# Performance work log

Measured on AMD Instinct MI355X. Metric: run time of the kernel, lower is better.

## Reference

```python
import jax, jax.numpy as jnp
import numpy as np

MAX_POS = 8192
SOFT_CAP = 5.0


def rms_norm(x, scale, eps=1e-6):
    # RMSBatchNorm approximated as RMS normalization over channels with learned scale
    return x * jax.lax.rsqrt(jnp.mean(x * x, axis=-1, keepdims=True) + eps) * scale


def layer_norm(x, scale, offset, eps=1e-5):
    mean = jnp.mean(x, axis=-1, keepdims=True)
    var = jnp.mean(jnp.square(x - mean), axis=-1, keepdims=True)
    return (x - mean) * jax.lax.rsqrt(var + eps) * scale + offset


def apply_rope(x, max_position=MAX_POS):
    # x: [B, S, H, C]
    B, S, H, C = x.shape
    positions = jnp.arange(S, dtype=x.dtype).reshape(1, S)
    num_freq = C // 2
    inv_freq = (1.0 / (jnp.arange(num_freq) + jnp.geomspace(1, max_position - num_freq + 1, num_freq))).astype(x.dtype)
    theta = jnp.einsum('bs,f->bsf', positions, inv_freq)
    theta = jnp.repeat(theta, 2, axis=-1)[..., None, :]  # [1, S, 1, C]
    x_rotated = jnp.stack([-x[..., 1::2], x[..., ::2]], axis=-1).reshape(x.shape)
    return x * jnp.cos(theta) + x_rotated * jnp.sin(theta)


def setup_inputs() -> dict:
    key = jax.random.key(0)
    ks = jax.random.split(key, 16)
    B, S, D = 2, 2048, 1536
    H, CQK, CV = 8, 128, 192
    inp = {
        'x': jax.random.normal(ks[0], (B, S, D), jnp.float32),
        'attention_bias': jax.random.normal(ks[1], (B, H, S, S), jnp.float32),
        'rms_in_scale': jnp.ones((D,), jnp.float32),
        'wq': jax.random.normal(ks[2], (D, H * CQK), jnp.float32) / np.sqrt(D),
        'wk': jax.random.normal(ks[3], (D, CQK), jnp.float32) / np.sqrt(D),
        'wv': jax.random.normal(ks[4], (D, CV), jnp.float32) / np.sqrt(D),
        'q_scale': jnp.ones((CQK,), jnp.float32),
        'q_offset': jnp.zeros((CQK,), jnp.float32),
        'k_scale': jnp.ones((CQK,), jnp.float32),
        'k_offset': jnp.zeros((CQK,), jnp.float32),
        'v_scale': jnp.ones((CV,), jnp.float32),
        'v_offset': jnp.zeros((CV,), jnp.float32),
        'wo': jax.random.normal(ks[5], (H * CV, D), jnp.float32) / np.sqrt(H * CV),
        'bo': jnp.zeros((D,), jnp.float32),
        'rms_out_scale': jnp.ones((D,), jnp.float32),
    }
    return inp


def reference(x, attention_bias, rms_in_scale, wq, wk, wv, q_scale, q_offset,
              k_scale, k_offset, v_scale, v_offset, wo, bo, rms_out_scale):
    B, S, D = x.shape
    H, CQK, CV = 8, 128, 192
    h = rms_norm(x, rms_in_scale)
    q = layer_norm((h @ wq).reshape(B, S, H, CQK), q_scale, q_offset)
    k = layer_norm((h @ wk).reshape(B, S, 1, CQK), k_scale, k_offset)
    v = layer_norm((h @ wv).reshape(B, S, 1, CV), v_scale, v_offset)
    q = apply_rope(q)
    k = apply_rope(k)
    # MQA logits: single shared K head
    logits = jnp.einsum('bshc,bSc->bhsS', q, k[:, :, 0], preferred_element_type=jnp.float32)
    logits = logits / np.sqrt(128.0)
    logits = (logits + attention_bias).astype(jnp.float32)
    logits = jnp.tanh(logits / SOFT_CAP) * SOFT_CAP
    weights = jax.nn.softmax(logits, axis=-1)
    y = jnp.einsum('bhsS,bSc->bshc', weights, v[:, :, 0]).astype(q.dtype)
    y = y.reshape(B, S, H * CV) @ wo + bo
    return rms_norm(y, rms_out_scale)
```

## Files before the change

### kernel.cpp

```cpp
#include <hip/hip_runtime.h>
#include <hip/hip_bf16.h>

typedef unsigned short u16;
typedef short bf16x8 __attribute__((ext_vector_type(8)));
typedef float f32x4 __attribute__((ext_vector_type(4)));

#define NB 2
#define NS 2048
#define ND 1536
#define NH 8
#define NCQK 128
#define NCV 192
#define NBS 4096
#define NPAD 1408

__device__ __forceinline__ float bf2f(u16 u) {
  unsigned v = ((unsigned)u) << 16;
  return __builtin_bit_cast(float, v);
}
__device__ __forceinline__ u16 f2bf(float f) {
  unsigned u = __builtin_bit_cast(unsigned, f);
  u += 0x7fffu + ((u >> 16) & 1u);
  return (u16)(u >> 16);
}
__device__ __forceinline__ void glds16(const u16* g, u16* l) {
  __builtin_amdgcn_global_load_lds(
      (const __attribute__((address_space(1))) void*)g,
      (__attribute__((address_space(3))) void*)l, 16, 0, 0);
}
__device__ __forceinline__ f32x4 mfma16(bf16x8 a, bf16x8 b, f32x4 c) {
  return __builtin_amdgcn_mfma_f32_16x16x32_bf16(a, b, c, 0, 0, 0);
}

__global__ void transpose_k(const float* __restrict__ in, u16* __restrict__ out,
                            int K, int N) {
  __shared__ float t[64][65];
  const int n0 = blockIdx.x * 64, k0 = blockIdx.y * 64;
  const int tid = threadIdx.x;
  const int rl = tid >> 4, cl = (tid & 15) * 4;
  for (int p = 0; p < 4; p++) {
    int k = rl + p * 16;
    float4 v = *(const float4*)(in + (size_t)(k0 + k) * N + n0 + cl);
    t[k][cl] = v.x; t[k][cl + 1] = v.y; t[k][cl + 2] = v.z; t[k][cl + 3] = v.w;
  }
  __syncthreads();
  const int rn = tid >> 3, ck = (tid & 7) * 8;
  for (int p = 0; p < 2; p++) {
    int n = rn + p * 32;
    u16 tmp[8];
    for (int j = 0; j < 8; j++) tmp[j] = f2bf(t[ck + j][n]);
    *(uint4*)(out + (size_t)(n0 + n) * K + k0 + ck) = *(uint4*)tmp;
  }
}

__global__ void rmsnorm_in_k(const float* __restrict__ x, const float* __restrict__ scale,
                             u16* __restrict__ h) {
  __shared__ float sbuf[4];
  const int row = blockIdx.x, tid = threadIdx.x;
  const float* xr = x + (size_t)row * ND;
  float v[6]; float ss = 0.f;
  for (int i = 0; i < 6; i++) { v[i] = xr[tid + i * 256]; ss += v[i] * v[i]; }
  for (int o = 32; o; o >>= 1) ss += __shfl_xor(ss, o);
  if ((tid & 63) == 0) sbuf[tid >> 6] = ss;
  __syncthreads();
  ss = sbuf[0] + sbuf[1] + sbuf[2] + sbuf[3];
  const float inv = rsqrtf(ss * (1.f / ND) + 1e-6f);
  u16* hr = h + (size_t)row * ND;
  for (int i = 0; i < 6; i++) {
    int c = tid + i * 256;
    hr[c] = f2bf(v[i] * inv * scale[c]);
  }
}

template <bool F32OUT>
__global__ __launch_bounds__(256, 2)
void gemm_nt(const u16* __restrict__ A, const u16* __restrict__ Bt,
             float* __restrict__ Cf, u16* __restrict__ Cb, int M, int N, int K) {
  __shared__ __align__(16) u16 As[128 * 64];
  __shared__ __align__(16) u16 Bs[128 * 64];
  const int tid = threadIdx.x;
  const int wave = tid >> 6, lane = tid & 63, quad = lane >> 4, l16 = lane & 15;
  const int m0 = blockIdx.y * 128, n0 = blockIdx.x * 128;
  const int mrb = (wave & 1) * 4, nrb = (wave >> 1) * 4;
  f32x4 acc[4][4] = {};
  for (int k0 = 0; k0 < K; k0 += 64) {
    if (k0) __syncthreads();
    for (int i = 0; i < 4; i++) {
      int g = wave * 4 + i;
      int rb = g >> 1, kh = g & 1;
      int row = rb * 16 + l16, kc = kh * 4 + quad;
      glds16(A + (size_t)(m0 + row) * K + k0 + kc * 8, &As[(rb * 8 + kh * 4) * 128]);
      glds16(Bt + (size_t)(n0 + row) * K + k0 + kc * 8, &Bs[(rb * 8 + kh * 4) * 128]);
    }
    __syncthreads();
    for (int kk = 0; kk < 2; kk++) {
      bf16x8 af[4], bfr[4];
      for (int f = 0; f < 4; f++)
        af[f] = *(const bf16x8*)&As[(((mrb + f) * 8 + kk * 4 + quad) * 16 + l16) * 8];
      for (int f = 0; f < 4; f++)
        bfr[f] = *(const bf16x8*)&Bs[(((nrb + f) * 8 + kk * 4 + quad) * 16 + l16) * 8];
      for (int mf = 0; mf < 4; mf++)
        for (int nf = 0; nf < 4; nf++)
          acc[mf][nf] = mfma16(af[mf], bfr[nf], acc[mf][nf]);
    }
  }
  for (int mf = 0; mf < 4; mf++)
    for (int nf = 0; nf < 4; nf++)
      for (int r = 0; r < 4; r++) {
        int m = m0 + (wave & 1) * 64 + mf * 16 + quad * 4 + r;
        int n = n0 + (wave >> 1) * 64 + nf * 16 + l16;
        if (F32OUT) Cf[(size_t)m * N + n] = acc[mf][nf][r];
        else        Cb[(size_t)m * N + n] = f2bf(acc[mf][nf][r]);
      }
}

__global__ void ln_rope_k(const float* __restrict__ qkv,
                          const float* __restrict__ qs, const float* __restrict__ qo,
                          const float* __restrict__ ks, const float* __restrict__ ko,
                          const float* __restrict__ vs, const float* __restrict__ vo,
                          u16* __restrict__ Qg, u16* __restrict__ Kg, u16* __restrict__ Vg) {
  const int row = blockIdx.x;
  const int b = row >> 11, s = row & (NS - 1);
  const int wave = threadIdx.x >> 6, lane = threadIdx.x & 63;
  const float* base = qkv + (size_t)row * NPAD;
  const float gsp = __expf(logf(8129.f) * ((float)lane * (1.f / 63.f)));
  const float invf = 1.f / ((float)lane + gsp);
  float sn, cs;
  sincosf((float)s * invf, &sn, &cs);

  for (int hh = 0; hh < 2; hh++) {
    const int h = wave * 2 + hh;
    const float* p = base + h * NCQK;
    float x0 = p[lane * 2], x1 = p[lane * 2 + 1];
    float s1 = x0 + x1, s2 = x0 * x0 + x1 * x1;
    for (int o = 32; o; o >>= 1) { s1 += __shfl_xor(s1, o); s2 += __shfl_xor(s2, o); }
    float mean = s1 * (1.f / NCQK);
    float inv = rsqrtf(s2 * (1.f / NCQK) - mean * mean + 1e-5f);
    float y0 = (x0 - mean) * inv * qs[lane * 2] + qo[lane * 2];
    float y1 = (x1 - mean) * inv * qs[lane * 2 + 1] + qo[lane * 2 + 1];
    u16* dst = Qg + (size_t)row * (NH * NCQK) + h * NCQK + lane * 2;
    dst[0] = f2bf(y0 * cs - y1 * sn);
    dst[1] = f2bf(y1 * cs + y0 * sn);
  }
  if (wave == 0) {
    const float* p = base + NH * NCQK;
    float x0 = p[lane * 2], x1 = p[lane * 2 + 1];
    float s1 = x0 + x1, s2 = x0 * x0 + x1 * x1;
    for (int o = 32; o; o >>= 1) { s1 += __shfl_xor(s1, o); s2 += __shfl_xor(s2, o); }
    float mean = s1 * (1.f / NCQK);
    float inv = rsqrtf(s2 * (1.f / NCQK) - mean * mean + 1e-5f);
    float y0 = (x0 - mean) * inv * ks[lane * 2] + ko[lane * 2];
    float y1 = (x1 - mean) * inv * ks[lane * 2 + 1] + ko[lane * 2 + 1];
    u16* dst = Kg + (size_t)row * NCQK + lane * 2;
    dst[0] = f2bf(y0 * cs - y1 * sn);
    dst[1] = f2bf(y1 * cs + y0 * sn);
  }
  if (wave == 1) {
    const float* p = base + NH * NCQK + NCQK;
    float x[3]; float s1 = 0.f, s2 = 0.f;
    for (int i = 0; i < 3; i++) { x[i] = p[lane + i * 64]; s1 += x[i]; s2 += x[i] * x[i]; }
    for (int o = 32; o; o >>= 1) { s1 += __shfl_xor(s1, o); s2 += __shfl_xor(s2, o); }
    float mean = s1 * (1.f / NCV);
    float inv = rsqrtf(s2 * (1.f / NCV) - mean * mean + 1e-5f);
    for (int i = 0; i < 3; i++) {
      int c = lane + i * 64;
      float y = (x[i] - mean) * inv * vs[c] + vo[c];
      Vg[(size_t)(b * NCV + c) * NS + s] = f2bf(y);
    }
  }
}

__global__ __launch_bounds__(256, 2)
void attn_k(const u16* __restrict__ Qg, const u16* __restrict__ Kg,
            const u16* __restrict__ Vg, const float* __restrict__ bias,
            u16* __restrict__ Y) {
  __shared__ __align__(16) u16 smem[24576];
  __shared__ float lbuf[64];
  u16* Ks = smem;
  u16* Vs = smem + 8192;
  u16* Ps = smem + 20480;
  const int tid = threadIdx.x;
  const int wave = tid >> 6, lane = tid & 63, quad = lane >> 4, l16 = lane & 15;
  const int pair = wave >> 1, rw = wave & 1;
  const int s0 = blockIdx.x * 64;
  const int h = blockIdx.y, b = blockIdx.z;

  const float C1 = 0.0510069742f;
  const float C2 = 0.5770780163f;
  const float C3 = -14.4269504089f;
  const float C4 = 7.2134752044f;

  bf16x8 qa[2][4];
#pragma unroll
  for (int mf = 0; mf < 2; mf++) {
    const u16* qr = Qg + ((size_t)((b * NS + s0 + rw * 32 + mf * 16 + l16) * NH + h)) * NCQK;
#pragma unroll
    for (int kk = 0; kk < 4; kk++)
      qa[mf][kk] = *(const bf16x8*)(qr + (kk * 4 + quad) * 8);
  }

  const u16* Kbase = Kg + (size_t)(b * NS) * NCQK;
  const u16* Vbase = Vg + (size_t)(b * NCV) * NS;
  const float* brow = bias + ((size_t)(b * NH + h) * NS + s0 + rw * 32) * NS + pair * 32 + l16;

#pragma unroll
  for (int i = 0; i < 4; i++)
    glds16(Kbase + (size_t)(wave * 16 + l16) * NCQK + (i * 4 + quad) * 8,
           &Ks[(wave * 16 + i * 4) * 128]);
#pragma unroll
  for (int i = 0; i < 6; i++) {
    int g = wave * 6 + i, cb = g >> 1, kh = g & 1;
    glds16(Vbase + (size_t)(cb * 16 + l16) * NS + (kh * 4 + quad) * 8,
           &Vs[(cb * 8 + kh * 4) * 128]);
  }
  float breg[16];
#pragma unroll
  for (int mf = 0; mf < 2; mf++)
#pragma unroll
    for (int nb = 0; nb < 2; nb++)
#pragma unroll
      for (int r = 0; r < 4; r++)
        breg[(mf * 2 + nb) * 4 + r] = brow[(size_t)(mf * 16 + quad * 4 + r) * NS + nb * 16];
  __syncthreads();

  f32x4 oacc[2][12] = {};
  float lsum[8] = {};

  const int pwb = wave * 1024;

  for (int kt = 0; kt < NS / 64; kt++) {
    f32x4 sacc[2][2] = {};
    __builtin_amdgcn_s_setprio(1);
#pragma unroll
    for (int kk = 0; kk < 4; kk++)
#pragma unroll
      for (int nb = 0; nb < 2; nb++) {
        bf16x8 kf = *(const bf16x8*)&Ks[(((pair * 2 + nb) * 16 + kk * 4 + quad) * 16 + l16) * 8];
        sacc[0][nb] = mfma16(qa[0][kk], kf, sacc[0][nb]);
        sacc[1][nb] = mfma16(qa[1][kk], kf, sacc[1][nb]);
      }
    __builtin_amdgcn_s_setprio(0);

#pragma unroll
    for (int mf = 0; mf < 2; mf++)
#pragma unroll
      for (int nb = 0; nb < 2; nb++) {
        const int xk = nb * 16 + l16;
#pragma unroll
        for (int r = 0; r < 4; r++) {
          float a = fmaf(sacc[mf][nb][r], C1, breg[(mf * 2 + nb) * 4 + r] * C2);
          float e2;
          asm("v_exp_f32 %0, %1" : "=v"(e2) : "v"(a));
          float u = __builtin_amdgcn_rcpf(e2 + 1.f);
          float a2 = fmaf(u, C3, C4);
          float p;
          asm("v_exp_f32 %0, %1" : "=v"(p) : "v"(a2));
          unsigned pk;
          asm("v_cvt_pk_bf16_f32 %0, %1, %2" : "=v"(pk) : "v"(p), "v"(p));
          lsum[mf * 4 + r] += __builtin_bit_cast(float, pk << 16);
          Ps[pwb + mf * 512 + (xk >> 3) * 128 + (quad * 4 + r) * 8 + (xk & 7)] = (u16)pk;
        }
      }

    if (kt + 1 < NS / 64) {
      const int key0 = (kt + 1) * 64;
#pragma unroll
      for (int mf = 0; mf < 2; mf++)
#pragma unroll
        for (int nb = 0; nb < 2; nb++)
#pragma unroll
          for (int r = 0; r < 4; r++)
            breg[(mf * 2 + nb) * 4 + r] = brow[(size_t)(mf * 16 + quad * 4 + r) * NS + key0 + nb * 16];
    }

    __builtin_amdgcn_s_setprio(1);
    bf16x8 pa0 = *(const bf16x8*)&Ps[pwb + quad * 128 + l16 * 8];
    bf16x8 pa1 = *(const bf16x8*)&Ps[pwb + 512 + quad * 128 + l16 * 8];
#pragma unroll
    for (int nb = 0; nb < 12; nb++) {
      bf16x8 vf = *(const bf16x8*)&Vs[((nb * 8 + pair * 4 + quad) * 16 + l16) * 8];
      oacc[0][nb] = mfma16(pa0, vf, oacc[0][nb]);
      oacc[1][nb] = mfma16(pa1, vf, oacc[1][nb]);
    }
    __builtin_amdgcn_s_setprio(0);

    if (kt + 1 < NS / 64) {
      const int key0 = (kt + 1) * 64;
      __syncthreads();
#pragma unroll
      for (int i = 0; i < 4; i++)
        glds16(Kbase + (size_t)(key0 + wave * 16 + l16) * NCQK + (i * 4 + quad) * 8,
               &Ks[(wave * 16 + i * 4) * 128]);
#pragma unroll
      for (int i = 0; i < 6; i++) {
        int g = wave * 6 + i, cb = g >> 1, kh = g & 1;
        glds16(Vbase + (size_t)(cb * 16 + l16) * NS + key0 + (kh * 4 + quad) * 8,
               &Vs[(cb * 8 + kh * 4) * 128]);
      }
      __syncthreads();
    }
  }

#pragma unroll
  for (int i = 0; i < 8; i++)
    for (int o = 1; o < 16; o <<= 1) lsum[i] += __shfl_xor(lsum[i], o);

  __syncthreads();
  float* smemF = (float*)smem;
  if (pair == 1) {
#pragma unroll
    for (int mf = 0; mf < 2; mf++) {
#pragma unroll
      for (int r = 0; r < 4; r++) {
        const int row = rw * 32 + mf * 16 + quad * 4 + r;
#pragma unroll
        for (int nb = 0; nb < 12; nb++)
          smemF[row * 192 + nb * 16 + l16] = oacc[mf][nb][r];
        if (l16 == 0) lbuf[row] = lsum[mf * 4 + r];
      }
    }
  }
  __syncthreads();
  if (pair == 0) {
#pragma unroll
    for (int mf = 0; mf < 2; mf++)
#pragma unroll
      for (int r = 0; r < 4; r++) {
        const int row = rw * 32 + mf * 16 + quad * 4 + r;
        const float inv = 1.f / (lsum[mf * 4 + r] + lbuf[row]);
        u16* yr = Y + (size_t)(b * NS + s0 + row) * ND + h * NCV;
#pragma unroll
        for (int nb = 0; nb < 12; nb++)
          yr[nb * 16 + l16] = f2bf((oacc[mf][nb][r] + smemF[row * 192 + nb * 16 + l16]) * inv);
      }
  }
}

__global__ void final_k(const u16* __restrict__ yo, const float* __restrict__ bo,
                        const float* __restrict__ scale, float* __restrict__ out) {
  __shared__ float sbuf[4];
  const int row = blockIdx.x, tid = threadIdx.x;
  const u16* yr = yo + (size_t)row * ND;
  float v[6]; float ss = 0.f;
  for (int i = 0; i < 6; i++) {
    int c = tid + i * 256;
    v[i] = bf2f(yr[c]) + bo[c];
    ss += v[i] * v[i];
  }
  for (int o = 32; o; o >>= 1) ss += __shfl_xor(ss, o);
  if ((tid & 63) == 0) sbuf[tid >> 6] = ss;
  __syncthreads();
  ss = sbuf[0] + sbuf[1] + sbuf[2] + sbuf[3];
  const float inv = rsqrtf(ss * (1.f / ND) + 1e-6f);
  float* orow = out + (size_t)row * ND;
  for (int i = 0; i < 6; i++) {
    int c = tid + i * 256;
    orow[c] = v[i] * inv * scale[c];
  }
}

extern "C" void kernel_launch(void* const* d_in, const int* in_sizes, int n_in,
                              void* d_out, int out_size, void* d_ws, size_t ws_size,
                              hipStream_t stream) {
  const float* x    = (const float*)d_in[0];
  const float* bias = (const float*)d_in[1];
  const float* rin  = (const float*)d_in[2];
  const float* wq   = (const float*)d_in[3];
  const float* wk   = (const float*)d_in[4];
  const float* wv   = (const float*)d_in[5];
  const float* qsc  = (const float*)d_in[6];
  const float* qof  = (const float*)d_in[7];
  const float* ksc  = (const float*)d_in[8];
  const float* kof  = (const float*)d_in[9];
  const float* vsc  = (const float*)d_in[10];
  const float* vof  = (const float*)d_in[11];
  const float* wo   = (const float*)d_in[12];
  const float* bo   = (const float*)d_in[13];
  const float* rout = (const float*)d_in[14];

  char* ws = (char*)d_ws;
  size_t off = 0;
  auto alloc = [&](size_t bytes) -> void* {
    void* p = ws + off;
    off += (bytes + 255) & ~(size_t)255;
    return p;
  };
  u16*   h    = (u16*)alloc((size_t)NBS * ND * 2);
  u16*   wtq  = (u16*)alloc((size_t)NPAD * ND * 2);
  u16*   wto  = (u16*)alloc((size_t)ND * ND * 2);
  float* qkv  = (float*)alloc((size_t)NBS * NPAD * 4);
  u16*   Qb   = (u16*)alloc((size_t)NBS * NH * NCQK * 2);
  u16*   Kb   = (u16*)alloc((size_t)NBS * NCQK * 2);
  u16*   Vtb  = (u16*)alloc((size_t)NB * NCV * NS * 2);
  u16*   Ybf  = (u16*)alloc((size_t)NBS * ND * 2);
  u16*   Yob  = (u16*)alloc((size_t)NBS * ND * 2);

  transpose_k<<<dim3(16, 24), 256, 0, stream>>>(wq, wtq, ND, 1024);
  transpose_k<<<dim3(2, 24), 256, 0, stream>>>(wk, wtq + (size_t)1024 * ND, ND, 128);
  transpose_k<<<dim3(3, 24), 256, 0, stream>>>(wv, wtq + (size_t)1152 * ND, ND, 192);
  transpose_k<<<dim3(24, 24), 256, 0, stream>>>(wo, wto, ND, ND);
  rmsnorm_in_k<<<NBS, 256, 0, stream>>>(x, rin, h);
  gemm_nt<true><<<dim3(NPAD / 128, NBS / 128), 256, 0, stream>>>(h, wtq, qkv, nullptr, NBS, NPAD, ND);
  ln_rope_k<<<NBS, 256, 0, stream>>>(qkv, qsc, qof, ksc, kof, vsc, vof, Qb, Kb, Vtb);
  attn_k<<<dim3(NS / 64, NH, NB), 256, 0, stream>>>(Qb, Kb, Vtb, bias, Ybf);
  gemm_nt<false><<<dim3(ND / 128, NBS / 128), 256, 0, stream>>>(Ybf, wto, nullptr, Yob, NBS, ND, ND);
  final_k<<<NBS, 256, 0, stream>>>(Yob, bo, rout, (float*)d_out);
}
```

Baseline: 585.9 us.

## Double-buffer GEMM LDS tiles and split K/V staging in attention loop

The GEMM kernel now uses two LDS buffers per operand, so the next K-tile is fetched while the current one is consumed, leaving one barrier per iteration instead of two. In the attention kernel, the next K tile and bias are staged right after the QK/softmax phase, overlapping the PV matmul. The next V tile is staged after the PV phase. The doubled GEMM LDS footprint (64KB per block) may reduce occupancy, and whether the async LDS writes are correctly fenced before they are read depends on glds16 semantics.

Result: no change. 583.6 us (-0.4%).

```diff
diff --git a/kernel.cpp b/kernel.cpp
--- a/kernel.cpp
+++ b/kernel.cpp
@@ -76,34 +76,49 @@
 __global__ __launch_bounds__(256, 2)
 void gemm_nt(const u16* __restrict__ A, const u16* __restrict__ Bt,
              float* __restrict__ Cf, u16* __restrict__ Cb, int M, int N, int K) {
-  __shared__ __align__(16) u16 As[128 * 64];
-  __shared__ __align__(16) u16 Bs[128 * 64];
+  __shared__ __align__(16) u16 As[2][64 * 128];
+  __shared__ __align__(16) u16 Bs[2][64 * 128];
   const int tid = threadIdx.x;
   const int wave = tid >> 6, lane = tid & 63, quad = lane >> 4, l16 = lane & 15;
   const int m0 = blockIdx.y * 128, n0 = blockIdx.x * 128;
   const int mrb = (wave & 1) * 4, nrb = (wave >> 1) * 4;
   f32x4 acc[4][4] = {};
-  for (int k0 = 0; k0 < K; k0 += 64) {
-    if (k0) __syncthreads();
+
+  auto stage = [&](int buf, int k0) {
+#pragma unroll
     for (int i = 0; i < 4; i++) {
       int g = wave * 4 + i;
       int rb = g >> 1, kh = g & 1;
       int row = rb * 16 + l16, kc = kh * 4 + quad;
-      glds16(A + (size_t)(m0 + row) * K + k0 + kc * 8, &As[(rb * 8 + kh * 4) * 128]);
-      glds16(Bt + (size_t)(n0 + row) * K + k0 + kc * 8, &Bs[(rb * 8 + kh * 4) * 128]);
-    }
-    __syncthreads();
+      glds16(A + (size_t)(m0 + row) * K + k0 + kc * 8, &As[buf][(rb * 8 + kh * 4) * 128]);
+      glds16(Bt + (size_t)(n0 + row) * K + k0 + kc * 8, &Bs[buf][(rb * 8 + kh * 4) * 128]);
+    }
+  };
+
+  const int nt = K >> 6;
+  stage(0, 0);
+  __syncthreads();
+  for (int t = 0; t < nt; t++) {
+    const int cur = t & 1;
+    if (t + 1 < nt) stage(cur ^ 1, (t + 1) * 64);
+#pragma unroll
     for (int kk = 0; kk < 2; kk++) {
       bf16x8 af[4], bfr[4];
+#pragma unroll
       for (int f = 0; f < 4; f++)
-        af[f] = *(const bf16x8*)&As[(((mrb + f) * 8 + kk * 4 + quad) * 16 + l16) * 8];
+        af[f] = *(const bf16x8*)&As[cur][(((mrb + f) * 8 + kk * 4 + quad) * 16 + l16) * 8];
+#pragma unroll
       for (int f = 0; f < 4; f++)
-        bfr[f] = *(const bf16x8*)&Bs[(((nrb + f) * 8 + kk * 4 + quad) * 16 + l16) * 8];
+        bfr[f] = *(const bf16x8*)&Bs[cur][(((nrb + f) * 8 + kk * 4 + quad) * 16 + l16) * 8];
+#pragma unroll
       for (int mf = 0; mf < 4; mf++)
+#pragma unroll
         for (int nf = 0; nf < 4; nf++)
           acc[mf][nf] = mfma16(af[mf], bfr[nf], acc[mf][nf]);
     }
-  }
+    __syncthreads();
+  }
+
   for (int mf = 0; mf < 4; mf++)
     for (int nf = 0; nf < 4; nf++)
       for (int r = 0; r < 4; r++) {
@@ -203,32 +218,44 @@
   const u16* Vbase = Vg + (size_t)(b * NCV) * NS;
   const float* brow = bias + ((size_t)(b * NH + h) * NS + s0 + rw * 32) * NS + pair * 32 + l16;
 
-#pragma unroll
-  for (int i = 0; i < 4; i++)
-    glds16(Kbase + (size_t)(wave * 16 + l16) * NCQK + (i * 4 + quad) * 8,
-           &Ks[(wave * 16 + i * 4) * 128]);
-#pragma unroll
-  for (int i = 0; i < 6; i++) {
-    int g = wave * 6 + i, cb = g >> 1, kh = g & 1;
-    glds16(Vbase + (size_t)(cb * 16 + l16) * NS + (kh * 4 + quad) * 8,
-           &Vs[(cb * 8 + kh * 4) * 128]);
-  }
+  auto stageK = [&](int key0) {
+#pragma unroll
+    for (int i = 0; i < 4; i++)
+      glds16(Kbase + (size_t)(key0 + wave * 16 + l16) * NCQK + (i * 4 + quad) * 8,
+             &Ks[(wave * 16 + i * 4) * 128]);
+  };
+  auto stageV = [&](int key0) {
+#pragma unroll
+    for (int i = 0; i < 6; i++) {
+      int g = wave * 6 + i, cb = g >> 1, kh = g & 1;
+      glds16(Vbase + (size_t)(cb * 16 + l16) * NS + key0 + (kh * 4 + quad) * 8,
+             &Vs[(cb * 8 + kh * 4) * 128]);
+    }
+  };
+
   float breg[16];
-#pragma unroll
-  for (int mf = 0; mf < 2; mf++)
-#pragma unroll
-    for (int nb = 0; nb < 2; nb++)
-#pragma unroll
-      for (int r = 0; r < 4; r++)
-        breg[(mf * 2 + nb) * 4 + r] = brow[(size_t)(mf * 16 + quad * 4 + r) * NS + nb * 16];
+  auto loadB = [&](int key0) {
+#pragma unroll
+    for (int mf = 0; mf < 2; mf++)
+#pragma unroll
+      for (int nb = 0; nb < 2; nb++)
+#pragma unroll
+        for (int r = 0; r < 4; r++)
+          breg[(mf * 2 + nb) * 4 + r] = brow[(size_t)(mf * 16 + quad * 4 + r) * NS + key0 + nb * 16];
+  };
+
+  stageK(0);
+  stageV(0);
+  loadB(0);
   __syncthreads();
 
   f32x4 oacc[2][12] = {};
   float lsum[8] = {};
 
   const int pwb = wave * 1024;
-
-  for (int kt = 0; kt < NS / 64; kt++) {
+  const int NT = NS / 64;
+
+  for (int kt = 0; kt < NT; kt++) {
     f32x4 sacc[2][2] = {};
     __builtin_amdgcn_s_setprio(1);
 #pragma unroll
@@ -262,15 +289,11 @@
         }
       }
 
-    if (kt + 1 < NS / 64) {
-      const int key0 = (kt + 1) * 64;
-#pragma unroll
-      for (int mf = 0; mf < 2; mf++)
-#pragma unroll
-        for (int nb = 0; nb < 2; nb++)
-#pragma unroll
-          for (int r = 0; r < 4; r++)
-            breg[(mf * 2 + nb) * 4 + r] = brow[(size_t)(mf * 16 + quad * 4 + r) * NS + key0 + nb * 16];
+    __syncthreads();
+
+    if (kt + 1 < NT) {
+      stageK((kt + 1) * 64);
+      loadB((kt + 1) * 64);
     }
 
     __builtin_amdgcn_s_setprio(1);
@@ -284,21 +307,9 @@
     }
     __builtin_amdgcn_s_setprio(0);
 
-    if (kt + 1 < NS / 64) {
-      const int key0 = (kt + 1) * 64;
-      __syncthreads();
-#pragma unroll
-      for (int i = 0; i < 4; i++)
-        glds16(Kbase + (size_t)(key0 + wave * 16 + l16) * NCQK + (i * 4 + quad) * 8,
-               &Ks[(wave * 16 + i * 4) * 128]);
-#pragma unroll
-      for (int i = 0; i < 6; i++) {
-        int g = wave * 6 + i, cb = g >> 1, kh = g & 1;
-        glds16(Vbase + (size_t)(cb * 16 + l16) * NS + key0 + (kh * 4 + quad) * 8,
-               &Vs[(cb * 8 + kh * 4) * 128]);
-      }
-      __syncthreads();
-    }
+    __syncthreads();
+
+    if (kt + 1 < NT) stageV((kt + 1) * 64);
   }
 
 #pragma unroll
```
